# Performance work log

Hardware: AMD Instinct MI355X
Metric: run time of the kernel (lower is better)

## Reference

```python
import jax, jax.numpy as jnp
import numpy as np

N_NODES = 100000


def _add_self_loops(edge_index, n):
    loop = jnp.arange(n, dtype=edge_index.dtype)
    src = jnp.concatenate([edge_index[0], loop])
    dst = jnp.concatenate([edge_index[1], loop])
    return src, dst


def _gcn_conv(x, W, b, src, dst, n):
    # h = X W, then symmetric-normalized scatter-add over edges (PyG GCNConv)
    h = x @ W
    ones = jnp.ones(src.shape[0], dtype=h.dtype)
    deg = jax.ops.segment_sum(ones, dst, num_segments=n)  # in-degree incl. self loops
    dinv = jnp.where(deg > 0, jax.lax.rsqrt(deg), 0.0)
    norm = dinv[src] * dinv[dst]                           # [E]
    msg = h[src] * norm[:, None]                           # gather + scale
    out = jax.ops.segment_sum(msg, dst, num_segments=n)    # scatter-add
    return out + b


def setup_inputs() -> dict:
    key = jax.random.key(0)
    k1, k2, k3, k4 = jax.random.split(key, 4)
    F, H, C = 128, 128, 16
    x = jax.random.normal(k1, (N_NODES, F), dtype=jnp.float32)
    edge_index = jax.random.randint(k2, (2, 1600000), 0, N_NODES, dtype=jnp.int64)
    W1 = jax.random.normal(k3, (F, H), dtype=jnp.float32) / np.sqrt(F)
    b1 = jnp.zeros((H,), dtype=jnp.float32)
    W2 = jax.random.normal(k4, (H, C), dtype=jnp.float32) / np.sqrt(H)
    b2 = jnp.zeros((C,), dtype=jnp.float32)
    return {"x": x, "edge_index": edge_index, "W1": W1, "b1": b1, "W2": W2, "b2": b2}


def reference(x, edge_index, W1, b1, W2, b2):
    n = x.shape[0]
    src, dst = _add_self_loops(edge_index, n)
    h = _gcn_conv(x, W1, b1, src, dst, n)
    h = jax.nn.relu(h)
    # dropout(p=0.1) treated as identity (deterministic eval-mode reference)
    logits = _gcn_conv(h, W2, b2, src, dst, n)
    return logits, jax.nn.log_softmax(logits, axis=1)
```

## Files before the change

kernel.cpp:

```cpp
#include <hip/hip_runtime.h>
#include <math.h>


#define ELLW 72
#define EPB 16384
#define BSH 9
#define MAXEB 100
#define MAXBK 200

typedef __attribute__((ext_vector_type(8))) short short8;
typedef __attribute__((ext_vector_type(4))) float f32x4;

__device__ __forceinline__ float bf2f(unsigned short u) {
    return __uint_as_float(((unsigned int)u) << 16);
}
__device__ __forceinline__ unsigned short f2bf(float f) {
    unsigned int u = __float_as_uint(f);
    unsigned int r = (u + 0x7fffu + ((u >> 16) & 1u)) >> 16;
    return (unsigned short)r;
}

__global__ void k_prep(unsigned short* __restrict__ h, float* __restrict__ g,
                       const float* __restrict__ W1, unsigned short* __restrict__ wt,
                       int n) {
    int i = blockIdx.x * blockDim.x + threadIdx.x;
    if (i < 16384) {
        int nc = i >> 7, k = i & 127;
        wt[i] = f2bf(W1[k * 128 + nc]);
    }
    if (i < 128) h[(size_t)n * 128 + i] = 0;
    if (i < 16) g[(size_t)n * 16 + i] = 0.f;
}

__global__ void k_hist(const int* __restrict__ dst, int E,
                       int* __restrict__ hist, int nbuck) {
    __shared__ int lh[MAXBK];
    const int t = threadIdx.x, blk = blockIdx.x;
    for (int i = t; i < nbuck; i += 256) lh[i] = 0;
    __syncthreads();
    const int e0 = blk * EPB;
    const int e1 = min(e0 + EPB, E);
    for (int e = e0 + t; e < e1; e += 256)
        atomicAdd(&lh[dst[e] >> BSH], 1);
    __syncthreads();
    for (int i = t; i < nbuck; i += 256)
        hist[blk * nbuck + i] = lh[i];
}

__global__ void k_scan(int* __restrict__ hist, int* __restrict__ bstart,
                       int* __restrict__ bcount, int neb, int nbuck) {
    __shared__ unsigned short lh[MAXEB * MAXBK];
    __shared__ int sc[256];
    const int t = threadIdx.x;
    const int items = neb * nbuck;
    for (int i = t; i < items; i += 256) lh[i] = (unsigned short)hist[i];
    __syncthreads();
    int total = 0;
    if (t < nbuck)
        for (int blk = 0; blk < neb; ++blk) total += lh[blk * nbuck + t];
    sc[t] = total;
    __syncthreads();
    for (int o = 1; o < 256; o <<= 1) {
        int x = 0;
        if (t >= o) x = sc[t - o];
        __syncthreads();
        if (t >= o) sc[t] += x;
        __syncthreads();
    }
    if (t < nbuck) {
        int run = sc[t] - total;
        bstart[t] = run;
        bcount[t] = total;
        for (int blk = 0; blk < neb; ++blk) {
            int idx = blk * nbuck + t;
            int v = lh[idx];
            hist[idx] = run;
            run += v;
        }
    }
}

__global__ void k_bin(const int* __restrict__ src, const int* __restrict__ dst, int E,
                      const int* __restrict__ hist, int* __restrict__ binned, int nbuck) {
    __shared__ int cnt[MAXBK];
    const int t = threadIdx.x, blk = blockIdx.x;
    for (int i = t; i < nbuck; i += 256) cnt[i] = hist[blk * nbuck + i];
    __syncthreads();
    const int e0 = blk * EPB;
    const int e1 = min(e0 + EPB, E);
    for (int e = e0 + t; e < e1; e += 256) {
        int d = dst[e];
        int b = d >> BSH;
        int pos = atomicAdd(&cnt[b], 1);
        binned[pos] = src[e] | ((d & ((1 << BSH) - 1)) << 17);
    }
}

__global__ void k_ell(const int* __restrict__ binned, const int* __restrict__ bstart,
                      const int* __restrict__ bcount, int* __restrict__ deg,
                      int* __restrict__ col, int n) {
    __shared__ int ldeg[1 << BSH];
    const int t = threadIdx.x, b = blockIdx.x;
    const int node0 = b << BSH;
    for (int i = t; i < (1 << BSH); i += 256) ldeg[i] = 0;
    __syncthreads();
    const int st = bstart[b], cv = bcount[b];
    for (int i = t; i < cv; i += 256) {
        int v = binned[st + i];
        int s = v & 0x1FFFF;
        int dl = v >> 17;
        int q = atomicAdd(&ldeg[dl], 1);
        if (q < ELLW) col[(size_t)(node0 + dl) * ELLW + q] = s;
    }
    __syncthreads();
    for (int i = t; i < (1 << BSH); i += 256) {
        int node = node0 + i;
        if (node < n) {
            int dgv = ldeg[i];
            deg[node] = dgv;
            int dc = dgv > ELLW ? ELLW : dgv;
            int kend = (dc + 7) & ~7;
            for (int q = dc; q < kend; ++q) col[(size_t)node * ELLW + q] = n;
        }
    }
}

__global__ void k_gemm1(const float* __restrict__ x, const unsigned short* __restrict__ wt,
                        const int* __restrict__ deg, unsigned short* __restrict__ h,
                        int n) {
    __shared__ unsigned short xs[64 * 136];
    const int t = threadIdx.x;
    const int row0 = blockIdx.x * 64;
    for (int i = t; i < 2048; i += 256) {
        int r = i >> 5, c4 = (i & 31) << 2;
        int gr = row0 + r;
        float4 v = make_float4(0.f, 0.f, 0.f, 0.f);
        if (gr < n) v = *(const float4*)(x + (size_t)gr * 128 + c4);
        ushort4 u;
        u.x = f2bf(v.x); u.y = f2bf(v.y); u.z = f2bf(v.z); u.w = f2bf(v.w);
        *(ushort4*)(xs + r * 136 + c4) = u;
    }
    __syncthreads();
    const int w = t >> 6;
    const int lane = t & 63;
    const int m = lane & 15, q = lane >> 4;
    f32x4 acc[8];
#pragma unroll
    for (int ns = 0; ns < 8; ++ns) acc[ns] = (f32x4){0.f, 0.f, 0.f, 0.f};
#pragma unroll
    for (int kt = 0; kt < 4; ++kt) {
        short8 a = *(const short8*)(xs + (w * 16 + m) * 136 + kt * 32 + q * 8);
#pragma unroll
        for (int ns = 0; ns < 8; ++ns) {
            short8 b = *(const short8*)((const short*)wt + (ns * 16 + m) * 128 + kt * 32 + q * 8);
            acc[ns] = __builtin_amdgcn_mfma_f32_16x16x32_bf16(a, b, acc[ns], 0, 0, 0);
        }
    }
    unsigned short* xsw = xs + (w * 16) * 136;
    float srow[4];
#pragma unroll
    for (int reg = 0; reg < 4; ++reg) {
        int gr = row0 + w * 16 + q * 4 + reg;
        srow[reg] = (gr < n) ? rsqrtf((float)(deg[gr] + 1)) : 0.f;
    }
#pragma unroll
    for (int ns = 0; ns < 8; ++ns)
#pragma unroll
        for (int reg = 0; reg < 4; ++reg)
            xsw[(q * 4 + reg) * 136 + ns * 16 + m] = f2bf(acc[ns][reg] * srow[reg]);
    __syncthreads();
#pragma unroll
    for (int it = 0; it < 8; ++it) {
        int rl = (lane >> 5) + it * 2;
        int off = (lane & 31) * 4;
        int gr = row0 + w * 16 + rl;
        if (gr < n)
            *(ushort4*)(h + (size_t)gr * 128 + off) = *(const ushort4*)(xsw + rl * 136 + off);
    }
}

__global__ __launch_bounds__(256, 2) void k_gather1f(
        const unsigned short* __restrict__ h, const int* __restrict__ deg,
        const int* __restrict__ col, const float* __restrict__ b1,
        const float* __restrict__ W2, float* __restrict__ g, int n) {
    const int t = threadIdx.x;
    const int lane = t & 15;
    const int d = blockIdx.x * 16 + (t >> 4);
    if (d >= n) return;
    int dg = deg[d];
    if (dg > ELLW) dg = ELLW;
    const float dd = rsqrtf((float)(dg + 1));
    const int kend = (dg + 7) & ~7;
    const int* ecol = col + (size_t)d * ELLW;

    float aA[8], aB[8];
    {
        short8 u = *(const short8*)(h + (size_t)d * 128 + lane * 8);
#pragma unroll
        for (int j = 0; j < 8; ++j) {
            aA[j] = bf2f((unsigned short)u[j]);
            aB[j] = 0.f;
        }
    }
    for (int k = 0; k < kend; k += 8) {
        int4 c0 = *(const int4*)(ecol + k);
        int4 c1 = *(const int4*)(ecol + k + 4);
        short8 u0 = *(const short8*)(h + (size_t)c0.x * 128 + lane * 8);
        short8 u1 = *(const short8*)(h + (size_t)c0.y * 128 + lane * 8);
        short8 u2 = *(const short8*)(h + (size_t)c0.z * 128 + lane * 8);
        short8 u3 = *(const short8*)(h + (size_t)c0.w * 128 + lane * 8);
        short8 u4 = *(const short8*)(h + (size_t)c1.x * 128 + lane * 8);
        short8 u5 = *(const short8*)(h + (size_t)c1.y * 128 + lane * 8);
        short8 u6 = *(const short8*)(h + (size_t)c1.z * 128 + lane * 8);
        short8 u7 = *(const short8*)(h + (size_t)c1.w * 128 + lane * 8);
#pragma unroll
        for (int j = 0; j < 8; ++j) {
            aA[j] += bf2f((unsigned short)u0[j]) + bf2f((unsigned short)u2[j]) +
                     bf2f((unsigned short)u4[j]) + bf2f((unsigned short)u6[j]);
            aB[j] += bf2f((unsigned short)u1[j]) + bf2f((unsigned short)u3[j]) +
                     bf2f((unsigned short)u5[j]) + bf2f((unsigned short)u7[j]);
        }
    }
    float y[8];
    const float* b1p = b1 + lane * 8;
#pragma unroll
    for (int j = 0; j < 8; ++j)
        y[j] = fmaxf(fmaf(aA[j] + aB[j], dd, b1p[j]), 0.f);
    const float4* w2v = (const float4*)(W2 + lane * 8 * 16);
    float4 z0 = make_float4(0.f, 0.f, 0.f, 0.f);
    float4 z1 = z0, z2 = z0, z3 = z0;
#pragma unroll
    for (int j = 0; j < 8; ++j) {
        float4 w0 = w2v[j * 4 + 0], w1 = w2v[j * 4 + 1];
        float4 w2 = w2v[j * 4 + 2], w3 = w2v[j * 4 + 3];
        float yj = y[j];
        z0.x = fmaf(yj, w0.x, z0.x); z0.y = fmaf(yj, w0.y, z0.y);
        z0.z = fmaf(yj, w0.z, z0.z); z0.w = fmaf(yj, w0.w, z0.w);
        z1.x = fmaf(yj, w1.x, z1.x); z1.y = fmaf(yj, w1.y, z1.y);
        z1.z = fmaf(yj, w1.z, z1.z); z1.w = fmaf(yj, w1.w, z1.w);
        z2.x = fmaf(yj, w2.x, z2.x); z2.y = fmaf(yj, w2.y, z2.y);
        z2.z = fmaf(yj, w2.z, z2.z); z2.w = fmaf(yj, w2.w, z2.w);
        z3.x = fmaf(yj, w3.x, z3.x); z3.y = fmaf(yj, w3.y, z3.y);
        z3.z = fmaf(yj, w3.z, z3.z); z3.w = fmaf(yj, w3.w, z3.w);
    }
#pragma unroll
    for (int mm = 1; mm < 16; mm <<= 1) {
        z0.x += __shfl_xor(z0.x, mm); z0.y += __shfl_xor(z0.y, mm);
        z0.z += __shfl_xor(z0.z, mm); z0.w += __shfl_xor(z0.w, mm);
        z1.x += __shfl_xor(z1.x, mm); z1.y += __shfl_xor(z1.y, mm);
        z1.z += __shfl_xor(z1.z, mm); z1.w += __shfl_xor(z1.w, mm);
        z2.x += __shfl_xor(z2.x, mm); z2.y += __shfl_xor(z2.y, mm);
        z2.z += __shfl_xor(z2.z, mm); z2.w += __shfl_xor(z2.w, mm);
        z3.x += __shfl_xor(z3.x, mm); z3.y += __shfl_xor(z3.y, mm);
        z3.z += __shfl_xor(z3.z, mm); z3.w += __shfl_xor(z3.w, mm);
    }
    if (lane < 4) {
        float4 z = (lane == 0) ? z0 : (lane == 1) ? z1 : (lane == 2) ? z2 : z3;
        z.x *= dd; z.y *= dd; z.z *= dd; z.w *= dd;
        *(float4*)(g + (size_t)d * 16 + lane * 4) = z;
    }
}

#define FACC(acc, v) \
    acc.x += v.x; acc.y += v.y; acc.z += v.z; acc.w += v.w

__global__ void k_gather2(const float* __restrict__ g, const int* __restrict__ deg,
                          const int* __restrict__ col, const float* __restrict__ b2,
                          float* __restrict__ out, int n) {
    const int t = threadIdx.x;
    const int d = blockIdx.x * 64 + (t >> 2);
    if (d >= n) return;
    const int l = t & 3;
    int dg = deg[d];
    if (dg > ELLW) dg = ELLW;
    const float dd = rsqrtf((float)(dg + 1));
    const int kend = (dg + 7) & ~7;
    const int* ecol = col + (size_t)d * ELLW;

    float4 aA = *(const float4*)(g + (size_t)d * 16 + l * 4);
    float4 aB = make_float4(0.f, 0.f, 0.f, 0.f);
    float4 aC = aB, aD = aB;
    for (int k = 0; k < kend; k += 8) {
        int4 c0 = *(const int4*)(ecol + k);
        int4 c1 = *(const int4*)(ecol + k + 4);
        float4 h0 = *(const float4*)(g + (size_t)c0.x * 16 + l * 4);
        float4 h1 = *(const float4*)(g + (size_t)c0.y * 16 + l * 4);
        float4 h2 = *(const float4*)(g + (size_t)c0.z * 16 + l * 4);
        float4 h3 = *(const float4*)(g + (size_t)c0.w * 16 + l * 4);
        float4 h4 = *(const float4*)(g + (size_t)c1.x * 16 + l * 4);
        float4 h5 = *(const float4*)(g + (size_t)c1.y * 16 + l * 4);
        float4 h6 = *(const float4*)(g + (size_t)c1.z * 16 + l * 4);
        float4 h7 = *(const float4*)(g + (size_t)c1.w * 16 + l * 4);
        FACC(aA, h0); FACC(aB, h1); FACC(aC, h2); FACC(aD, h3);
        FACC(aA, h4); FACC(aB, h5); FACC(aC, h6); FACC(aD, h7);
    }
    float4 bv = *(const float4*)(b2 + l * 4);
    float4 acc;
    acc.x = fmaf(aA.x + aB.x + aC.x + aD.x, dd, bv.x);
    acc.y = fmaf(aA.y + aB.y + aC.y + aD.y, dd, bv.y);
    acc.z = fmaf(aA.z + aB.z + aC.z + aD.z, dd, bv.z);
    acc.w = fmaf(aA.w + aB.w + aC.w + aD.w, dd, bv.w);
    *(float4*)(out + (size_t)d * 16 + l * 4) = acc;
    float m = fmaxf(fmaxf(acc.x, acc.y), fmaxf(acc.z, acc.w));
    m = fmaxf(m, __shfl_xor(m, 1));
    m = fmaxf(m, __shfl_xor(m, 2));
    float e = expf(acc.x - m) + expf(acc.y - m) + expf(acc.z - m) + expf(acc.w - m);
    e += __shfl_xor(e, 1);
    e += __shfl_xor(e, 2);
    float ls = m + logf(e);
    float4 o;
    o.x = acc.x - ls; o.y = acc.y - ls; o.z = acc.z - ls; o.w = acc.w - ls;
    *(float4*)(out + (size_t)n * 16 + (size_t)d * 16 + l * 4) = o;
}

static inline size_t align256(size_t v) { return (v + 255) & ~(size_t)255; }

extern "C" void kernel_launch(void* const* d_in, const int* in_sizes, int n_in,
                              void* d_out, int out_size, void* d_ws, size_t ws_size,
                              hipStream_t stream) {
    const float* x  = (const float*)d_in[0];
    const int*   ei = (const int*)d_in[1];
    const float* W1 = (const float*)d_in[2];
    const float* b1 = (const float*)d_in[3];
    const float* W2 = (const float*)d_in[4];
    const float* b2 = (const float*)d_in[5];
    float* out = (float*)d_out;

    const int n = in_sizes[0] / 128;
    const int E = in_sizes[1] / 2;
    const int* src = ei;
    const int* dst = ei + E;
    const int NEB = (E + EPB - 1) / EPB;
    const int NBUCK = (n + (1 << BSH) - 1) >> BSH;

    char* base = (char*)d_ws;
    size_t off = 0;
    int* deg = (int*)(base + off); off = align256(off + (size_t)n * 4);
    int* col = (int*)(base + off); off = align256(off + (size_t)n * ELLW * 4);
    unsigned short* wt = (unsigned short*)(base + off); off = align256(off + 128 * 128 * 2);
    unsigned short* h = (unsigned short*)(base + off); off = align256(off + ((size_t)n + 1) * 128 * 2);
    float* g = (float*)(base + off); off = align256(off + ((size_t)n + 1) * 16 * 4);
    int* hist = (int*)(base + off); off = align256(off + (size_t)MAXEB * MAXBK * 4);
    int* bstart = (int*)(base + off); off = align256(off + (size_t)MAXBK * 4);
    int* bcount = (int*)(base + off); off = align256(off + (size_t)MAXBK * 4);
    int* binned = (int*)(base + off); off = align256(off + (size_t)E * 4);

    k_prep<<<64, 256, 0, stream>>>(h, g, W1, wt, n);
    k_hist<<<NEB, 256, 0, stream>>>(dst, E, hist, NBUCK);
    k_scan<<<1, 256, 0, stream>>>(hist, bstart, bcount, NEB, NBUCK);
    k_bin<<<NEB, 256, 0, stream>>>(src, dst, E, hist, binned, NBUCK);
    k_ell<<<NBUCK, 256, 0, stream>>>(binned, bstart, bcount, deg, col, n);

    k_gemm1<<<(n + 63) / 64, 256, 0, stream>>>(x, wt, deg, h, n);
    k_gather1f<<<(n + 15) / 16, 256, 0, stream>>>(h, deg, col, b1, W2, g, n);

    k_gather2<<<(n + 63) / 64, 256, 0, stream>>>(g, deg, col, b2, out, n);
}
```

Baseline: 370.5 us.

## Store layer-2 features in fp16, merge prep with histogram, vectorize scan load

The intermediate g buffer (per-node 16-wide layer-2 features) is now stored as fp16 instead of fp32, which halves the bytes read by the random gathers in k_gather2. The prep kernel and the histogram kernel are merged into one launch, with the first 64 blocks doing prep, to remove a kernel launch. The scan kernel now loads the histogram as int4 vectors. The fp16 storage adds rounding error to the logits.

Result: faster. 351.4 us (-5.2%).

```diff
diff --git a/kernel.cpp b/kernel.cpp
--- a/kernel.cpp
+++ b/kernel.cpp
@@ -10,6 +10,8 @@
 
 typedef __attribute__((ext_vector_type(8))) short short8;
 typedef __attribute__((ext_vector_type(4))) float f32x4;
+typedef __attribute__((ext_vector_type(4))) int i32x4;
+typedef __attribute__((ext_vector_type(4))) _Float16 f16x4;
 
 __device__ __forceinline__ float bf2f(unsigned short u) {
     return __uint_as_float(((unsigned int)u) << 16);
@@ -19,23 +21,29 @@
     unsigned int r = (u + 0x7fffu + ((u >> 16) & 1u)) >> 16;
     return (unsigned short)r;
 }
-
-__global__ void k_prep(unsigned short* __restrict__ h, float* __restrict__ g,
-                       const float* __restrict__ W1, unsigned short* __restrict__ wt,
-                       int n) {
-    int i = blockIdx.x * blockDim.x + threadIdx.x;
-    if (i < 16384) {
-        int nc = i >> 7, k = i & 127;
-        wt[i] = f2bf(W1[k * 128 + nc]);
-    }
-    if (i < 128) h[(size_t)n * 128 + i] = 0;
-    if (i < 16) g[(size_t)n * 16 + i] = 0.f;
-}
-
-__global__ void k_hist(const int* __restrict__ dst, int E,
-                       int* __restrict__ hist, int nbuck) {
+__device__ __forceinline__ f32x4 h2f4(f16x4 v) {
+    f32x4 r;
+    r[0] = (float)v[0]; r[1] = (float)v[1]; r[2] = (float)v[2]; r[3] = (float)v[3];
+    return r;
+}
+
+__global__ void k_prep_hist(unsigned short* __restrict__ h, _Float16* __restrict__ g,
+                            const float* __restrict__ W1, unsigned short* __restrict__ wt,
+                            int n, const int* __restrict__ dst, int E,
+                            int* __restrict__ hist, int nbuck) {
     __shared__ int lh[MAXBK];
-    const int t = threadIdx.x, blk = blockIdx.x;
+    const int t = threadIdx.x;
+    if (blockIdx.x < 64) {
+        int i = blockIdx.x * 256 + t;
+        if (i < 16384) {
+            int nc = i >> 7, k = i & 127;
+            wt[i] = f2bf(W1[k * 128 + nc]);
+        }
+        if (i < 128) h[(size_t)n * 128 + i] = 0;
+        if (i < 16) g[(size_t)n * 16 + i] = (_Float16)0.f;
+        return;
+    }
+    const int blk = blockIdx.x - 64;
     for (int i = t; i < nbuck; i += 256) lh[i] = 0;
     __syncthreads();
     const int e0 = blk * EPB;
@@ -53,7 +61,16 @@
     __shared__ int sc[256];
     const int t = threadIdx.x;
     const int items = neb * nbuck;
-    for (int i = t; i < items; i += 256) lh[i] = (unsigned short)hist[i];
+    const int it4 = items >> 2;
+    for (int i = t; i < it4; i += 256) {
+        i32x4 v = *(const i32x4*)(hist + i * 4);
+        lh[i * 4 + 0] = (unsigned short)v[0];
+        lh[i * 4 + 1] = (unsigned short)v[1];
+        lh[i * 4 + 2] = (unsigned short)v[2];
+        lh[i * 4 + 3] = (unsigned short)v[3];
+    }
+    for (int i = (it4 << 2) + t; i < items; i += 256)
+        lh[i] = (unsigned short)hist[i];
     __syncthreads();
     int total = 0;
     if (t < nbuck)
@@ -182,7 +199,7 @@
 __global__ __launch_bounds__(256, 2) void k_gather1f(
         const unsigned short* __restrict__ h, const int* __restrict__ deg,
         const int* __restrict__ col, const float* __restrict__ b1,
-        const float* __restrict__ W2, float* __restrict__ g, int n) {
+        const float* __restrict__ W2, _Float16* __restrict__ g, int n) {
     const int t = threadIdx.x;
     const int lane = t & 15;
     const int d = blockIdx.x * 16 + (t >> 4);
@@ -256,15 +273,14 @@
     }
     if (lane < 4) {
         float4 z = (lane == 0) ? z0 : (lane == 1) ? z1 : (lane == 2) ? z2 : z3;
-        z.x *= dd; z.y *= dd; z.z *= dd; z.w *= dd;
-        *(float4*)(g + (size_t)d * 16 + lane * 4) = z;
-    }
-}
-
-#define FACC(acc, v) \
-    acc.x += v.x; acc.y += v.y; acc.z += v.z; acc.w += v.w
-
-__global__ void k_gather2(const float* __restrict__ g, const int* __restrict__ deg,
+        f16x4 zz;
+        zz[0] = (_Float16)(z.x * dd); zz[1] = (_Float16)(z.y * dd);
+        zz[2] = (_Float16)(z.z * dd); zz[3] = (_Float16)(z.w * dd);
+        *(f16x4*)(g + (size_t)d * 16 + lane * 4) = zz;
+    }
+}
+
+__global__ void k_gather2(const _Float16* __restrict__ g, const int* __restrict__ deg,
                           const int* __restrict__ col, const float* __restrict__ b2,
                           float* __restrict__ out, int n) {
     const int t = threadIdx.x;
@@ -276,41 +292,38 @@
     const float dd = rsqrtf((float)(dg + 1));
     const int kend = (dg + 7) & ~7;
     const int* ecol = col + (size_t)d * ELLW;
-
-    float4 aA = *(const float4*)(g + (size_t)d * 16 + l * 4);
-    float4 aB = make_float4(0.f, 0.f, 0.f, 0.f);
-    float4 aC = aB, aD = aB;
+    const _Float16* gl = g + l * 4;
+
+    f32x4 aA = h2f4(*(const f16x4*)(gl + (size_t)d * 16));
+    f32x4 aB = (f32x4){0.f, 0.f, 0.f, 0.f};
+    f32x4 aC = aB, aD = aB;
     for (int k = 0; k < kend; k += 8) {
         int4 c0 = *(const int4*)(ecol + k);
         int4 c1 = *(const int4*)(ecol + k + 4);
-        float4 h0 = *(const float4*)(g + (size_t)c0.x * 16 + l * 4);
-        float4 h1 = *(const float4*)(g + (size_t)c0.y * 16 + l * 4);
-        float4 h2 = *(const float4*)(g + (size_t)c0.z * 16 + l * 4);
-        float4 h3 = *(const float4*)(g + (size_t)c0.w * 16 + l * 4);
-        float4 h4 = *(const float4*)(g + (size_t)c1.x * 16 + l * 4);
-        float4 h5 = *(const float4*)(g + (size_t)c1.y * 16 + l * 4);
-        float4 h6 = *(const float4*)(g + (size_t)c1.z * 16 + l * 4);
-        float4 h7 = *(const float4*)(g + (size_t)c1.w * 16 + l * 4);
-        FACC(aA, h0); FACC(aB, h1); FACC(aC, h2); FACC(aD, h3);
-        FACC(aA, h4); FACC(aB, h5); FACC(aC, h6); FACC(aD, h7);
-    }
-    float4 bv = *(const float4*)(b2 + l * 4);
-    float4 acc;
-    acc.x = fmaf(aA.x + aB.x + aC.x + aD.x, dd, bv.x);
-    acc.y = fmaf(aA.y + aB.y + aC.y + aD.y, dd, bv.y);
-    acc.z = fmaf(aA.z + aB.z + aC.z + aD.z, dd, bv.z);
-    acc.w = fmaf(aA.w + aB.w + aC.w + aD.w, dd, bv.w);
-    *(float4*)(out + (size_t)d * 16 + l * 4) = acc;
-    float m = fmaxf(fmaxf(acc.x, acc.y), fmaxf(acc.z, acc.w));
+        f16x4 h0 = *(const f16x4*)(gl + (size_t)c0.x * 16);
+        f16x4 h1 = *(const f16x4*)(gl + (size_t)c0.y * 16);
+        f16x4 h2 = *(const f16x4*)(gl + (size_t)c0.z * 16);
+        f16x4 h3 = *(const f16x4*)(gl + (size_t)c0.w * 16);
+        f16x4 h4 = *(const f16x4*)(gl + (size_t)c1.x * 16);
+        f16x4 h5 = *(const f16x4*)(gl + (size_t)c1.y * 16);
+        f16x4 h6 = *(const f16x4*)(gl + (size_t)c1.z * 16);
+        f16x4 h7 = *(const f16x4*)(gl + (size_t)c1.w * 16);
+        aA += h2f4(h0); aB += h2f4(h1); aC += h2f4(h2); aD += h2f4(h3);
+        aA += h2f4(h4); aB += h2f4(h5); aC += h2f4(h6); aD += h2f4(h7);
+    }
+    f32x4 bv = *(const f32x4*)(b2 + l * 4);
+    f32x4 acc = (aA + aB + aC + aD) * dd + bv;
+    *(f32x4*)(out + (size_t)d * 16 + l * 4) = acc;
+    float m = fmaxf(fmaxf(acc[0], acc[1]), fmaxf(acc[2], acc[3]));
     m = fmaxf(m, __shfl_xor(m, 1));
     m = fmaxf(m, __shfl_xor(m, 2));
-    float e = expf(acc.x - m) + expf(acc.y - m) + expf(acc.z - m) + expf(acc.w - m);
+    float e = expf(acc[0] - m) + expf(acc[1] - m) + expf(acc[2] - m) + expf(acc[3] - m);
     e += __shfl_xor(e, 1);
     e += __shfl_xor(e, 2);
     float ls = m + logf(e);
-    float4 o;
-    o.x = acc.x - ls; o.y = acc.y - ls; o.z = acc.z - ls; o.w = acc.w - ls;
-    *(float4*)(out + (size_t)n * 16 + (size_t)d * 16 + l * 4) = o;
+    f32x4 o;
+    o[0] = acc[0] - ls; o[1] = acc[1] - ls; o[2] = acc[2] - ls; o[3] = acc[3] - ls;
+    *(f32x4*)(out + (size_t)n * 16 + (size_t)d * 16 + l * 4) = o;
 }
 
 static inline size_t align256(size_t v) { return (v + 255) & ~(size_t)255; }
@@ -339,14 +352,13 @@
     int* col = (int*)(base + off); off = align256(off + (size_t)n * ELLW * 4);
     unsigned short* wt = (unsigned short*)(base + off); off = align256(off + 128 * 128 * 2);
     unsigned short* h = (unsigned short*)(base + off); off = align256(off + ((size_t)n + 1) * 128 * 2);
-    float* g = (float*)(base + off); off = align256(off + ((size_t)n + 1) * 16 * 4);
+    _Float16* g = (_Float16*)(base + off); off = align256(off + ((size_t)n + 1) * 16 * 2);
     int* hist = (int*)(base + off); off = align256(off + (size_t)MAXEB * MAXBK * 4);
     int* bstart = (int*)(base + off); off = align256(off + (size_t)MAXBK * 4);
     int* bcount = (int*)(base + off); off = align256(off + (size_t)MAXBK * 4);
     int* binned = (int*)(base + off); off = align256(off + (size_t)E * 4);
 
-    k_prep<<<64, 256, 0, stream>>>(h, g, W1, wt, n);
-    k_hist<<<NEB, 256, 0, stream>>>(dst, E, hist, NBUCK);
+    k_prep_hist<<<64 + NEB, 256, 0, stream>>>(h, g, W1, wt, n, dst, E, hist, NBUCK);
     k_scan<<<1, 256, 0, stream>>>(hist, bstart, bcount, NEB, NBUCK);
     k_bin<<<NEB, 256, 0, stream>>>(src, dst, E, hist, binned, NBUCK);
     k_ell<<<NBUCK, 256, 0, stream>>>(binned, bstart, bcount, deg, col, n);
```
